# Optimization experiments

Measured on AMD Instinct MI355X. Metric: run time of the kernel, lower is better.

## Reference

```python
import jax, jax.numpy as jnp
import numpy as np

PRE_NMS_THRESH = 0.05
PRE_NMS_TOP_N = 1000
NMS_THRESH = 0.6
FPN_POST_NMS_TOP_N = 100
MIN_SIZE = 0
OFFSET = 10000.0  # per-class coordinate offset for batched per-class NMS
NEG = -1e9


def bilinear_resize(x, out_h, out_w):
    # x: [H, W, C] -> [out_h, out_w, C], matches torch interpolate(align_corners=False)
    H, W, _ = x.shape
    def grid(in_size, out_size):
        scale = in_size / out_size
        src = (jnp.arange(out_size, dtype=jnp.float32) + 0.5) * scale - 0.5
        src = jnp.clip(src, 0.0, in_size - 1.0)
        i0 = jnp.floor(src).astype(jnp.int32)
        i1 = jnp.minimum(i0 + 1, in_size - 1)
        lam = src - i0.astype(jnp.float32)
        return i0, i1, lam
    r0, r1, rl = grid(H, out_h)
    c0, c1, cl = grid(W, out_w)
    x = x[r0] * (1.0 - rl)[:, None, None] + x[r1] * rl[:, None, None]
    x = x[:, c0] * (1.0 - cl)[None, :, None] + x[:, c1] * cl[None, :, None]
    return x


def box_iou_plus1(b):
    area = (b[:, 2] - b[:, 0] + 1.0) * (b[:, 3] - b[:, 1] + 1.0)
    lt = jnp.maximum(b[:, None, :2], b[None, :, :2])
    rb = jnp.minimum(b[:, None, 2:], b[None, :, 2:])
    wh = jnp.clip(rb - lt + 1.0, 0.0)
    inter = wh[..., 0] * wh[..., 1]
    union = area[:, None] + area[None, :] - inter
    return inter / jnp.maximum(union, 1e-6)


def _forward(locations, box_cls, box_regression, centerness, box_mask, h, w):
    N, C, H, W = box_cls.shape
    M2 = box_mask.shape[1]
    Mi = int(np.sqrt(M2))
    HW = H * W
    K = PRE_NMS_TOP_N

    cls = jax.nn.sigmoid(box_cls.transpose(0, 2, 3, 1).reshape(N, HW, C))
    reg = box_regression.transpose(0, 2, 3, 1).reshape(N, HW, 4)
    cent = jax.nn.sigmoid(centerness.reshape(N, HW))
    mask = jax.nn.sigmoid(box_mask.transpose(0, 2, 3, 1))  # [N,H,W,M2]

    cand = cls > PRE_NMS_THRESH               # candidates from raw cls scores
    scr = cls * cent[:, :, None]              # centerness-weighted scores

    def per_image(cand_i, scr_i, reg_i, mask_i):
        # --- threshold + per-image topk (fixed K, padded with NEG) ---
        flat = jnp.where(cand_i, scr_i, NEG).reshape(HW * C)
        vals, idx = jax.lax.top_k(flat, K)
        valid = vals > NEG / 2
        loc_idx = idx // C
        labels = idx % C + 1                  # 1-based class labels
        locs = locations[loc_idx]             # [K,2]
        r = reg_i[loc_idx]                    # [K,4]
        boxes = jnp.stack([locs[:, 0] - r[:, 0], locs[:, 1] - r[:, 1],
                           locs[:, 0] + r[:, 2], locs[:, 1] + r[:, 3]], axis=1)
        scores = jnp.sqrt(jnp.where(valid, vals, 1.0)) * valid

        # --- mask paste: mean of upsampled mask over (buggy) box region ---
        up = bilinear_resize(mask_i, h, w)                      # [h,w,M2]
        integ = jnp.pad(jnp.cumsum(jnp.cumsum(up, 0), 1), ((1, 0), (1, 0), (0, 0)))
        bi = boxes.astype(jnp.int32)          # torch .int() truncation
        x1 = jnp.maximum(bi[:, 0], 0); x2 = jnp.minimum(bi[:, 2], h - 1)
        y1 = jnp.maximum(bi[:, 1], 0); y2 = jnp.minimum(bi[:, 3], w - 1)
        # original skip condition is (x1>=x2 or y1>=x2) -- bug replicated; extra
        # y1<y2 guard avoids NaN mean over empty region
        region_ok = (x1 < x2) & (y1 < x2) & (y1 < y2)
        x1c = jnp.clip(x1, 0, h); x2c = jnp.clip(x2, 0, h)
        y1c = jnp.clip(y1, 0, w); y2c = jnp.clip(y2, 0, w)
        s = integ[x2c, y2c] - integ[x1c, y2c] - integ[x2c, y1c] + integ[x1c, y1c]
        area = jnp.maximum((x2c - x1c) * (y2c - y1c), 1).astype(s.dtype)
        prob = ((s / area[:, None]) * region_ok[:, None]).reshape(K, Mi, Mi)

        # --- clip_to_image (x in [0,w-1], y in [0,h-1]) + remove_small_boxes ---
        bx = jnp.stack([jnp.clip(boxes[:, 0], 0, w - 1), jnp.clip(boxes[:, 1], 0, h - 1),
                        jnp.clip(boxes[:, 2], 0, w - 1), jnp.clip(boxes[:, 3], 0, h - 1)], 1)
        ws_ = bx[:, 2] - bx[:, 0] + 1.0
        hs_ = bx[:, 3] - bx[:, 1] + 1.0
        valid = valid & (ws_ >= MIN_SIZE) & (hs_ >= MIN_SIZE)

        # --- per-class greedy NMS via class-offset trick (fixed shape) ---
        nb = bx + (labels.astype(bx.dtype) * OFFSET)[:, None]
        order = jnp.argsort(-jnp.where(valid, scores, -1.0))
        nb_s, sc_s, v_s = nb[order], scores[order], valid[order]
        iou = box_iou_plus1(nb_s)
        rng = jnp.arange(K)
        def step(keep, i):
            ki = keep[i] & v_s[i]
            keep = keep.at[i].set(ki)
            keep = keep & ~(ki & (iou[i] > NMS_THRESH) & (rng > i))
            return keep, None
        keep, _ = jax.lax.scan(step, jnp.ones(K, bool), jnp.arange(K))
        v_final = keep & v_s

        # --- keep fpn_post_nms_top_n highest-scoring survivors ---
        fvals, fidx = jax.lax.top_k(jnp.where(v_final, sc_s, -1.0), FPN_POST_NMS_TOP_N)
        sel = order[fidx]
        vfin = v_final[fidx]
        return (bx[sel], scores[sel] * vfin, labels[sel], prob[sel] * vfin[:, None, None], vfin)

    return jax.vmap(per_image)(cand, scr, reg, mask)


def setup_inputs() -> dict:
    key = jax.random.key(0)
    ks = jax.random.split(key, 4)
    N, C, H, W, M2 = 2, 80, 32, 40, 196
    stride = 8
    ys, xs = jnp.meshgrid(jnp.arange(H), jnp.arange(W), indexing='ij')
    locations = jnp.stack([xs.reshape(-1), ys.reshape(-1)], 1).astype(jnp.float32) * stride + stride // 2
    box_cls = jax.random.normal(ks[0], (N, C, H, W), jnp.float32) - 2.0
    box_regression = jax.random.uniform(ks[1], (N, 4, H, W), jnp.float32) * 60.0 + 4.0
    centerness = jax.random.normal(ks[2], (N, 1, H, W), jnp.float32)
    box_mask = jax.random.normal(ks[3], (N, M2, H, W), jnp.float32)
    return {"locations": locations, "box_cls": box_cls, "box_regression": box_regression,
            "centerness": centerness, "box_mask": box_mask, "image_h": 256, "image_w": 320}


def reference(locations, box_cls, box_regression, centerness, box_mask, image_h, image_w):
    return _forward(locations, box_cls, box_regression, centerness, box_mask, image_h, image_w)
```

## Files before the change

kernel.cpp:

```cpp
#include <hip/hip_runtime.h>

#define DEVI __device__ __forceinline__

constexpr int N_ = 2, C_ = 80, H_ = 32, W_ = 40, HW_ = H_ * W_, HWC_ = HW_ * C_;
constexpr int KTOP = 1000, M2_ = 196;
constexpr int IMH = 256, IMW = 320;
constexpr int NB = 2048;
constexpr int KB = 16;
constexpr int SLICE = HWC_ / KB;
constexpr int BCAP = 2048;
constexpr int GCAP = 4096;

constexpr int O_SC = 800, O_LB = 1000, O_PB = 1200, O_VF = 40400;

DEVI unsigned long long mapd(double v) {
  unsigned long long u = (unsigned long long)__double_as_longlong(v);
  return (u & 0x8000000000000000ull) ? ~u : (u | 0x8000000000000000ull);
}
DEVI double unmapd(unsigned long long k) {
  unsigned long long u = (k & 0x8000000000000000ull) ? (k ^ 0x8000000000000000ull) : ~k;
  return __longlong_as_double((long long)u);
}
DEVI int i0of(int x, int cap) {
  float src = ((float)x + 0.5f) * 0.125f - 0.5f;
  src = fminf(fmaxf(src, 0.f), (float)cap);
  return (int)floorf(src);
}

__global__ __launch_bounds__(1024) void k_pre(const float* cls, const float* cent, const float* bm,
                                              unsigned* ghist, float* msig, float* wr, float* wc) {
  int b = blockIdx.x, tid = threadIdx.x;
  if (b < N_ * KB) {
    __shared__ unsigned hist[NB];
    __shared__ float ce[HW_];
    int n = b >> 4, sb = b & 15;
    size_t base = (size_t)n * HWC_ + (size_t)sb * SLICE;
    for (int j = tid; j < NB; j += 1024) hist[j] = 0;
    for (int j = tid; j < HW_; j += 1024) ce[j] = 1.f / (1.f + expf(-cent[n * HW_ + j]));
    __syncthreads();
    #pragma unroll
    for (int it = 0; it < 7; ++it) {
      int j = it * 1024 + tid;
      if (j < SLICE) {
        float aa = cls[base + j];
        float s = 1.f / (1.f + expf(-aa));
        if (s > 0.0499999f) {
          unsigned key = __float_as_uint(s * ce[j % HW_]);
          int bin = (int)(key >> 16) - 0x3800;
          bin = bin < 0 ? 0 : (bin > NB - 1 ? NB - 1 : bin);
          atomicAdd(&hist[bin], 1u);
        }
      }
    }
    __syncthreads();
    unsigned* gh = ghist + ((size_t)n * KB + sb) * NB;
    for (int j = tid; j < NB; j += 1024) gh[j] = hist[j];
  } else if (b < N_ * KB + 140) {
    __shared__ float tile[4][32][33];
    int g = tid >> 8, sub = tid & 255;
    int tt = (b - N_ * KB) * 4 + g;
    int n = tt / 280, r = tt % 280, rqt = r / 7, ct = r % 7;
    int tx = sub & 31, ty = sub >> 5;
    int rq0 = rqt * 32, c0 = ct * 32;
    for (int i = 0; i < 4; ++i) {
      int cc = c0 + ty + i * 8, rq = rq0 + tx;
      if (cc < M2_) {
        float v = bm[((size_t)n * M2_ + cc) * HW_ + rq];
        tile[g][ty + i * 8][tx] = 1.f / (1.f + expf(-v));
      }
    }
    __syncthreads();
    for (int i = 0; i < 4; ++i) {
      int rq = rq0 + ty + i * 8, cc = c0 + tx;
      if (cc < M2_) msig[((size_t)n * HW_ + rq) * M2_ + cc] = tile[g][tx][ty + i * 8];
    }
  } else {
    int t = tid;
    if (t < H_) {
      int r = t; float acc = 0.f; wr[0 * H_ + r] = 0.f;
      for (int x = 0; x < IMH; ++x) {
        float src = ((float)x + 0.5f) * ((float)H_ / (float)IMH) - 0.5f;
        src = fminf(fmaxf(src, 0.f), (float)(H_ - 1));
        int i0 = (int)floorf(src); int i1 = min(i0 + 1, H_ - 1);
        float lam = src - (float)i0;
        float w = ((r == i0) ? (1.f - lam) : 0.f) + ((r == i1) ? lam : 0.f);
        acc += w; wr[(x + 1) * H_ + r] = acc;
      }
    } else if (t < H_ + W_) {
      int q = t - H_; float acc = 0.f; wc[0 * W_ + q] = 0.f;
      for (int y = 0; y < IMW; ++y) {
        float src = ((float)y + 0.5f) * ((float)W_ / (float)IMW) - 0.5f;
        src = fminf(fmaxf(src, 0.f), (float)(W_ - 1));
        int i0 = (int)floorf(src); int i1 = min(i0 + 1, W_ - 1);
        float lam = src - (float)i0;
        float w = ((q == i0) ? (1.f - lam) : 0.f) + ((q == i1) ? lam : 0.f);
        acc += w; wc[(y + 1) * W_ + q] = acc;
      }
    }
  }
}

__global__ __launch_bounds__(1024) void k_compact(const unsigned* ghist, const float* cls, const float* cent,
                                                  unsigned long long* bufK, unsigned* bufI, unsigned* cntG) {
  __shared__ unsigned wtot[16], wabove[16], sliceCnt[16], sliceOff[17];
  __shared__ unsigned sD, lcnt;
  __shared__ float ce[HW_];
  int b = blockIdx.x, n = b >> 4, sb = b & 15;
  int tid = threadIdx.x, lane = tid & 63, wid = tid >> 6;
  for (int j = tid; j < HW_; j += 1024) ce[j] = 1.f / (1.f + expf(-cent[n * HW_ + j]));
  const unsigned* gh = ghist + (size_t)n * KB * NB;
  unsigned a = 0, bv = 0;
  #pragma unroll
  for (int q = 0; q < KB; ++q) { a += gh[q * NB + 2 * tid]; bv += gh[q * NB + 2 * tid + 1]; }
  if (tid == 0) { sD = 0; lcnt = 0; }
  unsigned s2 = a + bv, suf = s2;
  for (int off = 1; off < 64; off <<= 1) {
    unsigned v = __shfl_down(suf, off);
    if (lane + off < 64) suf += v;
  }
  if (lane == 0) wtot[wid] = suf;
  __syncthreads();
  if (tid == 0) { unsigned acc = 0; for (int w = 15; w >= 0; --w) { wabove[w] = acc; acc += wtot[w]; } }
  __syncthreads();
  unsigned above = (suf - s2) + wabove[wid];
  if (above < 1000u && above + bv >= 1000u) sD = (unsigned)(2 * tid + 1);
  if (above + bv < 1000u && above + bv + a >= 1000u) sD = (unsigned)(2 * tid);
  __syncthreads();
  unsigned D = sD;
  unsigned Dg = (D > 0) ? D - 1 : 0;
  {
    unsigned acc = 0;
    for (int bin = (int)Dg + lane; bin < NB; bin += 64) acc += gh[wid * NB + bin];
    for (int off = 32; off; off >>= 1) acc += __shfl_down(acc, off);
    if (lane == 0) sliceCnt[wid] = acc;
  }
  __syncthreads();
  if (tid == 0) {
    unsigned acc = 0;
    for (int q = 0; q < KB; ++q) { sliceOff[q] = acc; acc += sliceCnt[q]; }
    sliceOff[KB] = acc;
    if (sb == 0) cntG[n] = acc;
  }
  __syncthreads();
  unsigned myStart = sliceOff[sb];
  size_t gbase = (size_t)n * HWC_ + (size_t)sb * SLICE;
  for (int it = 0; it < 7; ++it) {
    int j = it * 1024 + tid;
    bool win = false; float aa = 0.f;
    if (j < SLICE) {
      aa = cls[gbase + j];
      float s = 1.f / (1.f + expf(-aa));
      if (s > 0.0499999f) {
        unsigned key = __float_as_uint(s * ce[j % HW_]);
        int bin = (int)(key >> 16) - 0x3800;
        bin = bin < 0 ? 0 : (bin > NB - 1 ? NB - 1 : bin);
        win = ((unsigned)bin >= Dg);
      }
    }
    unsigned long long mb = __ballot(win);
    if (mb) {
      int lead = __builtin_ctzll(mb);
      unsigned offw = 0;
      if (lane == lead) offw = atomicAdd(&lcnt, (unsigned)__popcll(mb));
      offw = (unsigned)__shfl((int)offw, lead);
      if (win) {
        unsigned pos = myStart + offw + (unsigned)__popcll(mb & ((1ull << lane) - 1ull));
        if (pos < (unsigned)GCAP) {
          int hw = j % HW_, c = sb * 5 + j / HW_;
          double ss = 1.0 / (1.0 + exp(-(double)aa));
          double ced = 1.0 / (1.0 + exp(-(double)cent[n * HW_ + hw]));
          double v = (ss > 0.05) ? ss * ced : -1e9;
          bufK[(size_t)n * GCAP + pos] = mapd(v);
          bufI[(size_t)n * GCAP + pos] = (unsigned)(hw * C_ + c);
        }
      }
    }
  }
}

struct RankSh {
  unsigned long long K[BCAP];
  unsigned I[BCAP];
  unsigned short eb[BCAP];
  unsigned short ord[BCAP];
  unsigned bh[NB], bs[NB], cur[NB];
  unsigned long long Ks[1024];
  unsigned Is[1024];
  unsigned wtot[16], wabove[16];
};

__global__ __launch_bounds__(1024) void k_rankdec(const unsigned long long* bufK, const unsigned* bufI,
                                                  const unsigned* cntG, const float* loc, const float* breg,
                                                  double* bxd, double* scd, int* lab, int* vld, int* rg,
                                                  unsigned* keepg) {
  __shared__ RankSh sh;
  int n = blockIdx.x, tid = threadIdx.x, lane = tid & 63, wid = tid >> 6;
  keepg[n * 1024 + tid] = 0;
  int G = (int)cntG[n]; if (G > BCAP) G = BCAP;
  for (int j = tid; j < NB; j += 1024) sh.bh[j] = 0;
  for (int p = tid; p < G; p += 1024) {
    sh.K[p] = bufK[(size_t)n * GCAP + p];
    sh.I[p] = bufI[(size_t)n * GCAP + p];
  }
  __syncthreads();
  for (int p = tid; p < G; p += 1024) {
    double v = unmapd(sh.K[p]);
    int bb = 0;
    if (v > 0.0) {
      unsigned kb = __float_as_uint((float)v);
      bb = (int)(kb >> 16) - 0x3800;
      bb = bb < 0 ? 0 : (bb > NB - 1 ? NB - 1 : bb);
    }
    sh.eb[p] = (unsigned short)bb;
    atomicAdd(&sh.bh[bb], 1u);
  }
  __syncthreads();
  {
    unsigned a2 = sh.bh[2 * tid], b2 = sh.bh[2 * tid + 1];
    unsigned s3 = a2 + b2, suf2 = s3;
    for (int off = 1; off < 64; off <<= 1) {
      unsigned v = __shfl_down(suf2, off);
      if (lane + off < 64) suf2 += v;
    }
    if (lane == 0) sh.wtot[wid] = suf2;
    __syncthreads();
    if (tid == 0) { unsigned acc = 0; for (int w = 15; w >= 0; --w) { sh.wabove[w] = acc; acc += sh.wtot[w]; } }
    __syncthreads();
    unsigned above2 = (suf2 - s3) + sh.wabove[wid];
    sh.bs[2 * tid + 1] = above2;  sh.cur[2 * tid + 1] = above2;
    sh.bs[2 * tid] = above2 + b2; sh.cur[2 * tid] = above2 + b2;
  }
  __syncthreads();
  for (int p = tid; p < G; p += 1024) {
    unsigned p2 = atomicAdd(&sh.cur[sh.eb[p]], 1u);
    sh.ord[p2] = (unsigned short)p;
  }
  __syncthreads();
  for (int p = tid; p < G; p += 1024) {
    int bb = sh.eb[p];
    unsigned lo = sh.bs[bb], len = sh.bh[bb];
    unsigned long long k1 = sh.K[p]; unsigned i1 = sh.I[p];
    unsigned r = lo;
    for (unsigned q = lo; q < lo + len; ++q) {
      int j = sh.ord[q];
      unsigned long long kj = sh.K[j]; unsigned ij = sh.I[j];
      if ((kj > k1) || (kj == k1 && ij < i1)) ++r;
    }
    if (r < 1024u) { sh.Ks[r] = k1; sh.Is[r] = i1; }
  }
  for (int j = G + tid; j < 1024; j += 1024) { sh.Ks[j] = 0ull; sh.Is[j] = 0xFFFFFFFFu; }
  __syncthreads();
  if (tid < KTOP) {
    unsigned long long key = sh.Ks[tid];
    unsigned idx = sh.Is[tid];
    double v = unmapd(key);
    int valid = (v > -5e8) && (idx < (unsigned)HWC_);
    if (idx >= (unsigned)HWC_) idx = 0;
    int hw = (int)(idx / C_), c = (int)(idx % C_);
    double lx = (double)loc[hw * 2 + 0], ly = (double)loc[hw * 2 + 1];
    const float* rg4 = breg + (size_t)n * 4 * HW_;
    double r0 = (double)rg4[0 * HW_ + hw], r1 = (double)rg4[1 * HW_ + hw];
    double r2 = (double)rg4[2 * HW_ + hw], r3 = (double)rg4[3 * HW_ + hw];
    double b0 = lx - r0, b1 = ly - r1, b2 = lx + r2, b3 = ly + r3;
    double sc = valid ? sqrt(v) : 0.0;
    int bi0 = (int)b0, bi1 = (int)b1, bi2 = (int)b2, bi3 = (int)b3;
    int x1 = max(bi0, 0), x2 = min(bi2, IMH - 1), y1 = max(bi1, 0), y2 = min(bi3, IMW - 1);
    int rok = (x1 < x2) && (y1 < x2) && (y1 < y2);
    int x1c = min(max(x1, 0), IMH), x2c = min(max(x2, 0), IMH);
    int y1c = min(max(y1, 0), IMW), y2c = min(max(y2, 0), IMW);
    int area = max((x2c - x1c) * (y2c - y1c), 1);
    double c0 = fmin(fmax(b0, 0.0), (double)(IMW - 1));
    double c1 = fmin(fmax(b1, 0.0), (double)(IMH - 1));
    double c2 = fmin(fmax(b2, 0.0), (double)(IMW - 1));
    double c3 = fmin(fmax(b3, 0.0), (double)(IMH - 1));
    size_t base = (size_t)n * 1024 + tid;
    bxd[base * 4 + 0] = c0; bxd[base * 4 + 1] = c1; bxd[base * 4 + 2] = c2; bxd[base * 4 + 3] = c3;
    scd[base] = sc; lab[base] = c + 1; vld[base] = valid;
    int* r8 = rg + base * 8;
    r8[0] = x1c; r8[1] = x2c; r8[2] = y1c; r8[3] = y2c; r8[4] = area; r8[5] = rok;
  }
}

__global__ void k_nms(const double* bxd, const int* lab, const int* vld, unsigned* keepg) {
  int cls = blockIdx.x + 1, n = blockIdx.y, tid = threadIdx.x;
  __shared__ int mk[KTOP];
  __shared__ double mb0[KTOP], mb1[KTOP], mb2[KTOP], mb3[KTOP], ma[KTOP];
  __shared__ unsigned char kept[KTOP];
  int m = 0;
  for (int base = 0; base < KTOP; base += 64) {
    int t = base + tid;
    bool pred = (t < KTOP) && (lab[n * 1024 + t] == cls) && (vld[n * 1024 + t] != 0);
    unsigned long long bb = __ballot(pred);
    if (pred) {
      int pos = m + (int)__popcll(bb & ((1ull << tid) - 1ull));
      mk[pos] = t;
      const double* p = bxd + ((size_t)n * 1024 + t) * 4;
      double b0 = p[0], b1 = p[1], b2 = p[2], b3 = p[3];
      mb0[pos] = b0; mb1[pos] = b1; mb2[pos] = b2; mb3[pos] = b3;
      ma[pos] = (b2 - b0 + 1.0) * (b3 - b1 + 1.0);
      kept[pos] = 1;
    }
    m += (int)__popcll(bb);
  }
  __syncthreads();
  for (int i = 0; i < m; ++i) {
    if (kept[i]) {
      double x1 = mb0[i], y1 = mb1[i], x2 = mb2[i], y2 = mb3[i], ai = ma[i];
      for (int j = i + 1 + tid; j < m; j += 64) {
        double ltx = fmax(x1, mb0[j]), lty = fmax(y1, mb1[j]);
        double rbx = fmin(x2, mb2[j]), rby = fmin(y2, mb3[j]);
        double iw = fmax(rbx - ltx + 1.0, 0.0), ih = fmax(rby - lty + 1.0, 0.0);
        double inter = iw * ih;
        double uni = ai + ma[j] - inter;
        if (inter / fmax(uni, 1e-6) > 0.6) kept[j] = 0;
      }
    }
    __syncthreads();
  }
  for (int i = tid; i < m; i += 64) keepg[n * 1024 + mk[i]] = (unsigned)kept[i];
}

__global__ __launch_bounds__(256) void k_finish(const unsigned* keepg, const double* bxd,
                                                const double* scd, const int* lab, const int* rg,
                                                const float* msig, const float* wr, const float* wc,
                                                float* out) {
  int t = blockIdx.x, n = blockIdx.y, tid = threadIdx.x, lane = tid & 63, wid = tid >> 6;
  __shared__ int lsel[100], lvf[100];
  __shared__ unsigned woff[4]; __shared__ unsigned sS;
  __shared__ float A[H_], B[W_];

  int i0 = tid * 4;
  unsigned ff[4]; int lc = 0;
  for (int j = 0; j < 4; ++j) {
    int i = i0 + j;
    ff[j] = (i < KTOP) ? keepg[n * 1024 + i] : 0u;
    lc += (int)ff[j];
  }
  unsigned pre = (unsigned)lc;
  for (int off = 1; off < 64; off <<= 1) {
    unsigned v = __shfl_up(pre, off);
    if (lane >= off) pre += v;
  }
  if (lane == 63) woff[wid] = pre;
  __syncthreads();
  if (tid == 0) { unsigned acc = 0; for (int w = 0; w < 4; ++w) { unsigned tmp = woff[w]; woff[w] = acc; acc += tmp; } sS = acc; }
  __syncthreads();
  int kpre = (int)(woff[wid] + pre - (unsigned)lc);
  int S = (int)sS;
  for (int j = 0; j < 4; ++j) {
    int i = i0 + j;
    if (i < KTOP) {
      if (ff[j]) { if (kpre < 100) { lsel[kpre] = i; lvf[kpre] = 1; } kpre++; }
      else { int slot = S + (i - kpre); if (slot < 100) { lsel[slot] = i; lvf[slot] = 0; } }
    }
  }
  __syncthreads();

  int k = lsel[t], vf = lvf[t];
  if (tid == 0) {
    const double* bb = bxd + ((size_t)n * 1024 + k) * 4;
    out[(n * 100 + t) * 4 + 0] = (float)bb[0];
    out[(n * 100 + t) * 4 + 1] = (float)bb[1];
    out[(n * 100 + t) * 4 + 2] = (float)bb[2];
    out[(n * 100 + t) * 4 + 3] = (float)bb[3];
    out[O_SC + n * 100 + t] = vf ? (float)scd[n * 1024 + k] : 0.f;
    out[O_LB + n * 100 + t] = (float)lab[n * 1024 + k];
    out[O_VF + n * 100 + t] = (float)vf;
  }
  const int* r8 = rg + ((size_t)n * 1024 + k) * 8;
  int x1c = r8[0], x2c = r8[1], y1c = r8[2], y2c = r8[3], area = r8[4], rok = r8[5];
  if (tid < H_) A[tid] = wr[x2c * H_ + tid] - wr[x1c * H_ + tid];
  else if (tid < H_ + W_) { int q = tid - H_; B[q] = wc[y2c * W_ + q] - wc[y1c * W_ + q]; }
  __syncthreads();
  if (tid < M2_) {
    float acc = 0.f;
    if (rok && vf) {
      int rlo = i0of(x1c, H_ - 1);
      int rhi = min(i0of(x2c - 1, H_ - 1) + 1, H_ - 1);
      int qlo = i0of(y1c, W_ - 1);
      int qhi = min(i0of(y2c - 1, W_ - 1) + 1, W_ - 1);
      for (int r = rlo; r <= rhi; ++r) {
        float ar = A[r];
        const float* mrow = msig + ((size_t)((n * H_ + r) * W_ + qlo)) * M2_ + tid;
        float rs = 0.f;
        #pragma unroll 4
        for (int q = qlo; q <= qhi; ++q) { rs += B[q] * mrow[0]; mrow += M2_; }
        acc += ar * rs;
      }
      acc /= (float)area;
    }
    out[O_PB + (size_t)(n * 100 + t) * M2_ + tid] = acc;
  }
}

extern "C" void kernel_launch(void* const* d_in, const int* in_sizes, int n_in,
                              void* d_out, int out_size, void* d_ws, size_t ws_size,
                              hipStream_t stream) {
  (void)in_sizes; (void)n_in; (void)out_size; (void)ws_size;
  const float* locations = (const float*)d_in[0];
  const float* box_cls   = (const float*)d_in[1];
  const float* box_reg   = (const float*)d_in[2];
  const float* cent      = (const float*)d_in[3];
  const float* box_mask  = (const float*)d_in[4];
  float* out = (float*)d_out;

  char* ws = (char*)d_ws;
  size_t off = 0;
  auto alloc = [&](size_t bytes) -> void* {
    void* p = ws + off;
    off = (off + bytes + 255) & ~(size_t)255;
    return p;
  };
  unsigned* ghist          = (unsigned*)alloc((size_t)N_ * KB * NB * 4);
  unsigned long long* bufK = (unsigned long long*)alloc((size_t)N_ * GCAP * 8);
  unsigned* bufI           = (unsigned*)alloc((size_t)N_ * GCAP * 4);
  unsigned* cntG           = (unsigned*)alloc(16 * 4);
  double* bxd              = (double*)alloc((size_t)N_ * 1024 * 4 * 8);
  double* scd              = (double*)alloc((size_t)N_ * 1024 * 8);
  int* lab                 = (int*)alloc((size_t)N_ * 1024 * 4);
  int* vld                 = (int*)alloc((size_t)N_ * 1024 * 4);
  int* rg                  = (int*)alloc((size_t)N_ * 1024 * 8 * 4);
  unsigned* keepg          = (unsigned*)alloc((size_t)N_ * 1024 * 4);
  float* msig              = (float*)alloc((size_t)N_ * HW_ * M2_ * 4);
  float* wr                = (float*)alloc((size_t)(IMH + 1) * H_ * 4);
  float* wc                = (float*)alloc((size_t)(IMW + 1) * W_ * 4);

  k_pre<<<N_ * KB + 140 + 1, 1024, 0, stream>>>(box_cls, cent, box_mask, ghist, msig, wr, wc);
  k_compact<<<N_ * KB, 1024, 0, stream>>>(ghist, box_cls, cent, bufK, bufI, cntG);
  k_rankdec<<<N_, 1024, 0, stream>>>(bufK, bufI, cntG, locations, box_reg,
                                     bxd, scd, lab, vld, rg, keepg);
  k_nms<<<dim3(C_, N_), 64, 0, stream>>>(bxd, lab, vld, keepg);
  k_finish<<<dim3(100, N_), 256, 0, stream>>>(keepg, bxd, scd, lab, rg, msig, wr, wc, out);
}
```

Baseline: 91.70 us.

## Merge five kernels into two using inter-block flag barriers

Fuses histogram, compaction and rank/decode into one kernel whose blocks synchronize through global spin-wait flags instead of kernel boundaries. NMS and the finishing mask-pooling stage are merged into a second kernel, also using flags. This removes three kernel launches and their gaps. The cost is spin-waiting that depends on all cooperating blocks being co-resident, plus flag reset bookkeeping that could deadlock or race if residency or ordering assumptions fail.

```diff
diff --git a/kernel.cpp b/kernel.cpp
--- a/kernel.cpp
+++ b/kernel.cpp
@@ -10,6 +10,7 @@
 constexpr int SLICE = HWC_ / KB;
 constexpr int BCAP = 2048;
 constexpr int GCAP = 4096;
+constexpr unsigned MAGIC = 0x5EEDFACEu;
 
 constexpr int O_SC = 800, O_LB = 1000, O_PB = 1200, O_VF = 40400;
 
@@ -27,36 +28,229 @@
   return (int)floorf(src);
 }
 
-__global__ __launch_bounds__(1024) void k_pre(const float* cls, const float* cent, const float* bm,
-                                              unsigned* ghist, float* msig, float* wr, float* wc) {
-  int b = blockIdx.x, tid = threadIdx.x;
+DEVI unsigned aload(unsigned* p) { return atomicAdd(p, 0u); }
+
+struct SliceSh {
+  unsigned hist[NB];
+  float ce[HW_];
+  unsigned wtot[16], wabove[16], sliceCnt[16], sliceOff[17];
+  unsigned sD, lcnt;
+};
+struct RankSh {
+  unsigned long long K[BCAP];
+  unsigned I[BCAP];
+  unsigned short eb[BCAP];
+  unsigned short ord[BCAP];
+  unsigned bh[NB], bs[NB], cur[NB];
+  unsigned long long Ks[1024];
+  unsigned Is[1024];
+  unsigned wtot[16], wabove[16];
+};
+struct MaskSh { float tile[4][32][33]; };
+union ShA { SliceSh s; RankSh r; MaskSh m; };
+
+__global__ __launch_bounds__(1024) void k_a(const float* cls, const float* cent, const float* bm,
+                                            const float* loc, const float* breg,
+                                            unsigned* ghist, unsigned long long* bufK, unsigned* bufI,
+                                            double* bxd, double* scd, int* lab, int* vld, int* rg,
+                                            unsigned* keepg, float* msig, float* wr, float* wc,
+                                            unsigned* flags) {
+  __shared__ ShA sh;
+  int b = blockIdx.x, tid = threadIdx.x, lane = tid & 63, wid = tid >> 6;
+
   if (b < N_ * KB) {
-    __shared__ unsigned hist[NB];
-    __shared__ float ce[HW_];
     int n = b >> 4, sb = b & 15;
-    size_t base = (size_t)n * HWC_ + (size_t)sb * SLICE;
-    for (int j = tid; j < NB; j += 1024) hist[j] = 0;
-    for (int j = tid; j < HW_; j += 1024) ce[j] = 1.f / (1.f + expf(-cent[n * HW_ + j]));
+    size_t gbase = (size_t)n * HWC_ + (size_t)sb * SLICE;
+    for (int j = tid; j < NB; j += 1024) sh.s.hist[j] = 0;
+    for (int j = tid; j < HW_; j += 1024) sh.s.ce[j] = 1.f / (1.f + expf(-cent[n * HW_ + j]));
     __syncthreads();
     #pragma unroll
     for (int it = 0; it < 7; ++it) {
       int j = it * 1024 + tid;
       if (j < SLICE) {
-        float aa = cls[base + j];
+        float aa = cls[gbase + j];
         float s = 1.f / (1.f + expf(-aa));
         if (s > 0.0499999f) {
-          unsigned key = __float_as_uint(s * ce[j % HW_]);
+          unsigned key = __float_as_uint(s * sh.s.ce[j % HW_]);
           int bin = (int)(key >> 16) - 0x3800;
           bin = bin < 0 ? 0 : (bin > NB - 1 ? NB - 1 : bin);
-          atomicAdd(&hist[bin], 1u);
+          atomicAdd(&sh.s.hist[bin], 1u);
         }
       }
     }
     __syncthreads();
     unsigned* gh = ghist + ((size_t)n * KB + sb) * NB;
-    for (int j = tid; j < NB; j += 1024) gh[j] = hist[j];
+    for (int j = tid; j < NB; j += 1024) gh[j] = sh.s.hist[j];
+    __threadfence();
+    if (tid == 0) atomicExch(&flags[n * 16 + sb], MAGIC);
+    if (tid == 0) { for (int q = 0; q < 16; ++q) while (aload(&flags[n * 16 + q]) != MAGIC) {} }
+    __syncthreads();
+    __threadfence();
+    {
+      const unsigned* ghn = ghist + (size_t)n * KB * NB;
+      unsigned a = 0, bv = 0;
+      #pragma unroll
+      for (int q = 0; q < KB; ++q) { a += ghn[q * NB + 2 * tid]; bv += ghn[q * NB + 2 * tid + 1]; }
+      if (tid == 0) { sh.s.sD = 0; sh.s.lcnt = 0; }
+      unsigned s2 = a + bv, suf = s2;
+      for (int off = 1; off < 64; off <<= 1) {
+        unsigned v = __shfl_down(suf, off);
+        if (lane + off < 64) suf += v;
+      }
+      if (lane == 0) sh.s.wtot[wid] = suf;
+      __syncthreads();
+      if (tid == 0) { unsigned acc = 0; for (int w = 15; w >= 0; --w) { sh.s.wabove[w] = acc; acc += sh.s.wtot[w]; } }
+      __syncthreads();
+      unsigned above = (suf - s2) + sh.s.wabove[wid];
+      if (above < 1000u && above + bv >= 1000u) sh.s.sD = (unsigned)(2 * tid + 1);
+      if (above + bv < 1000u && above + bv + a >= 1000u) sh.s.sD = (unsigned)(2 * tid);
+      __syncthreads();
+      unsigned D = sh.s.sD;
+      unsigned Dg = (D > 0) ? D - 1 : 0;
+      {
+        unsigned acc = 0;
+        for (int bin = (int)Dg + lane; bin < NB; bin += 64) acc += ghn[wid * NB + bin];
+        for (int off = 32; off; off >>= 1) acc += __shfl_down(acc, off);
+        if (lane == 0) sh.s.sliceCnt[wid] = acc;
+      }
+      __syncthreads();
+      if (tid == 0) {
+        unsigned acc = 0;
+        for (int q = 0; q < KB; ++q) { sh.s.sliceOff[q] = acc; acc += sh.s.sliceCnt[q]; }
+        sh.s.sliceOff[KB] = acc;
+      }
+      __syncthreads();
+      unsigned myStart = sh.s.sliceOff[sb];
+      for (int it = 0; it < 7; ++it) {
+        int j = it * 1024 + tid;
+        bool win = false; float aa = 0.f;
+        if (j < SLICE) {
+          aa = cls[gbase + j];
+          float s = 1.f / (1.f + expf(-aa));
+          if (s > 0.0499999f) {
+            unsigned key = __float_as_uint(s * sh.s.ce[j % HW_]);
+            int bin = (int)(key >> 16) - 0x3800;
+            bin = bin < 0 ? 0 : (bin > NB - 1 ? NB - 1 : bin);
+            win = ((unsigned)bin >= Dg);
+          }
+        }
+        unsigned long long mb = __ballot(win);
+        if (mb) {
+          int lead = __builtin_ctzll(mb);
+          unsigned offw = 0;
+          if (lane == lead) offw = atomicAdd(&sh.s.lcnt, (unsigned)__popcll(mb));
+          offw = (unsigned)__shfl((int)offw, lead);
+          if (win) {
+            unsigned pos = myStart + offw + (unsigned)__popcll(mb & ((1ull << lane) - 1ull));
+            if (pos < (unsigned)GCAP) {
+              int hw = j % HW_, c = sb * 5 + j / HW_;
+              double ss = 1.0 / (1.0 + exp(-(double)aa));
+              double ced = 1.0 / (1.0 + exp(-(double)cent[n * HW_ + hw]));
+              double v = (ss > 0.05) ? ss * ced : -1e9;
+              bufK[(size_t)n * GCAP + pos] = mapd(v);
+              bufI[(size_t)n * GCAP + pos] = (unsigned)(hw * C_ + c);
+            }
+          }
+        }
+      }
+    }
+    int G = (int)sh.s.sliceOff[KB];
+    __threadfence();
+    if (tid == 0) atomicExch(&flags[32 + n * 16 + sb], MAGIC);
+    if (sb != 0) return;
+    if (tid == 0) { for (int q = 0; q < 16; ++q) while (aload(&flags[32 + n * 16 + q]) != MAGIC) {} }
+    __syncthreads();
+    __threadfence();
+    if (G > BCAP) G = BCAP;
+    for (int j = tid; j < NB; j += 1024) sh.r.bh[j] = 0;
+    for (int p = tid; p < G; p += 1024) {
+      sh.r.K[p] = bufK[(size_t)n * GCAP + p];
+      sh.r.I[p] = bufI[(size_t)n * GCAP + p];
+    }
+    __syncthreads();
+    for (int p = tid; p < G; p += 1024) {
+      double v = unmapd(sh.r.K[p]);
+      int bb = 0;
+      if (v > 0.0) {
+        unsigned kb = __float_as_uint((float)v);
+        bb = (int)(kb >> 16) - 0x3800;
+        bb = bb < 0 ? 0 : (bb > NB - 1 ? NB - 1 : bb);
+      }
+      sh.r.eb[p] = (unsigned short)bb;
+      atomicAdd(&sh.r.bh[bb], 1u);
+    }
+    __syncthreads();
+    {
+      unsigned a2 = sh.r.bh[2 * tid], b2 = sh.r.bh[2 * tid + 1];
+      unsigned s3 = a2 + b2, suf2 = s3;
+      for (int off = 1; off < 64; off <<= 1) {
+        unsigned v = __shfl_down(suf2, off);
+        if (lane + off < 64) suf2 += v;
+      }
+      if (lane == 0) sh.r.wtot[wid] = suf2;
+      __syncthreads();
+      if (tid == 0) { unsigned acc = 0; for (int w = 15; w >= 0; --w) { sh.r.wabove[w] = acc; acc += sh.r.wtot[w]; } }
+      __syncthreads();
+      unsigned above2 = (suf2 - s3) + sh.r.wabove[wid];
+      sh.r.bs[2 * tid + 1] = above2;  sh.r.cur[2 * tid + 1] = above2;
+      sh.r.bs[2 * tid] = above2 + b2; sh.r.cur[2 * tid] = above2 + b2;
+    }
+    __syncthreads();
+    for (int p = tid; p < G; p += 1024) {
+      unsigned p2 = atomicAdd(&sh.r.cur[sh.r.eb[p]], 1u);
+      sh.r.ord[p2] = (unsigned short)p;
+    }
+    __syncthreads();
+    for (int p = tid; p < G; p += 1024) {
+      int bb = sh.r.eb[p];
+      unsigned lo = sh.r.bs[bb], len = sh.r.bh[bb];
+      unsigned long long k1 = sh.r.K[p]; unsigned i1 = sh.r.I[p];
+      unsigned r = lo;
+      for (unsigned q = lo; q < lo + len; ++q) {
+        int j = sh.r.ord[q];
+        unsigned long long kj = sh.r.K[j]; unsigned ij = sh.r.I[j];
+        if ((kj > k1) || (kj == k1 && ij < i1)) ++r;
+      }
+      if (r < 1024u) { sh.r.Ks[r] = k1; sh.r.Is[r] = i1; }
+    }
+    for (int j = G + tid; j < 1024; j += 1024) { sh.r.Ks[j] = 0ull; sh.r.Is[j] = 0xFFFFFFFFu; }
+    __syncthreads();
+    if (tid < KTOP) {
+      unsigned long long key = sh.r.Ks[tid];
+      unsigned idx = sh.r.Is[tid];
+      double v = unmapd(key);
+      int valid = (v > -5e8) && (idx < (unsigned)HWC_);
+      if (idx >= (unsigned)HWC_) idx = 0;
+      int hw = (int)(idx / C_), c = (int)(idx % C_);
+      double lx = (double)loc[hw * 2 + 0], ly = (double)loc[hw * 2 + 1];
+      const float* rg4 = breg + (size_t)n * 4 * HW_;
+      double r0 = (double)rg4[0 * HW_ + hw], r1 = (double)rg4[1 * HW_ + hw];
+      double r2 = (double)rg4[2 * HW_ + hw], r3 = (double)rg4[3 * HW_ + hw];
+      double b0 = lx - r0, b1 = ly - r1, b2 = lx + r2, b3 = ly + r3;
+      double sc = valid ? sqrt(v) : 0.0;
+      int bi0 = (int)b0, bi1 = (int)b1, bi2 = (int)b2, bi3 = (int)b3;
+      int x1 = max(bi0, 0), x2 = min(bi2, IMH - 1), y1 = max(bi1, 0), y2 = min(bi3, IMW - 1);
+      int rok = (x1 < x2) && (y1 < x2) && (y1 < y2);
+      int x1c = min(max(x1, 0), IMH), x2c = min(max(x2, 0), IMH);
+      int y1c = min(max(y1, 0), IMW), y2c = min(max(y2, 0), IMW);
+      int area = max((x2c - x1c) * (y2c - y1c), 1);
+      double c0 = fmin(fmax(b0, 0.0), (double)(IMW - 1));
+      double c1 = fmin(fmax(b1, 0.0), (double)(IMH - 1));
+      double c2 = fmin(fmax(b2, 0.0), (double)(IMW - 1));
+      double c3 = fmin(fmax(b3, 0.0), (double)(IMH - 1));
+      size_t base = (size_t)n * 1024 + tid;
+      bxd[base * 4 + 0] = c0; bxd[base * 4 + 1] = c1; bxd[base * 4 + 2] = c2; bxd[base * 4 + 3] = c3;
+      scd[base] = sc; lab[base] = c + 1; vld[base] = valid;
+      int* r8 = rg + base * 8;
+      r8[0] = x1c; r8[1] = x2c; r8[2] = y1c; r8[3] = y2c; r8[4] = area; r8[5] = rok;
+    }
+    for (int j = tid; j < 1024; j += 1024) keepg[n * 1024 + j] = 0;
+    __syncthreads();
+    if (tid == 0) {
+      flags[64 + n] = 0;
+      for (int q = 0; q < 16; ++q) { flags[n * 16 + q] = 0; flags[32 + n * 16 + q] = 0; }
+    }
   } else if (b < N_ * KB + 140) {
-    __shared__ float tile[4][32][33];
     int g = tid >> 8, sub = tid & 255;
     int tt = (b - N_ * KB) * 4 + g;
     int n = tt / 280, r = tt % 280, rqt = r / 7, ct = r % 7;
@@ -66,13 +260,13 @@
       int cc = c0 + ty + i * 8, rq = rq0 + tx;
       if (cc < M2_) {
         float v = bm[((size_t)n * M2_ + cc) * HW_ + rq];
-        tile[g][ty + i * 8][tx] = 1.f / (1.f + expf(-v));
+        sh.m.tile[g][ty + i * 8][tx] = 1.f / (1.f + expf(-v));
       }
     }
     __syncthreads();
     for (int i = 0; i < 4; ++i) {
       int rq = rq0 + ty + i * 8, cc = c0 + tx;
-      if (cc < M2_) msig[((size_t)n * HW_ + rq) * M2_ + cc] = tile[g][tx][ty + i * 8];
+      if (cc < M2_) msig[((size_t)n * HW_ + rq) * M2_ + cc] = sh.m.tile[g][tx][ty + i * 8];
     }
   } else {
     int t = tid;
@@ -100,296 +294,144 @@
   }
 }
 
-__global__ __launch_bounds__(1024) void k_compact(const unsigned* ghist, const float* cls, const float* cent,
-                                                  unsigned long long* bufK, unsigned* bufI, unsigned* cntG) {
-  __shared__ unsigned wtot[16], wabove[16], sliceCnt[16], sliceOff[17];
-  __shared__ unsigned sD, lcnt;
-  __shared__ float ce[HW_];
-  int b = blockIdx.x, n = b >> 4, sb = b & 15;
-  int tid = threadIdx.x, lane = tid & 63, wid = tid >> 6;
-  for (int j = tid; j < HW_; j += 1024) ce[j] = 1.f / (1.f + expf(-cent[n * HW_ + j]));
-  const unsigned* gh = ghist + (size_t)n * KB * NB;
-  unsigned a = 0, bv = 0;
-  #pragma unroll
-  for (int q = 0; q < KB; ++q) { a += gh[q * NB + 2 * tid]; bv += gh[q * NB + 2 * tid + 1]; }
-  if (tid == 0) { sD = 0; lcnt = 0; }
-  unsigned s2 = a + bv, suf = s2;
-  for (int off = 1; off < 64; off <<= 1) {
-    unsigned v = __shfl_down(suf, off);
-    if (lane + off < 64) suf += v;
-  }
-  if (lane == 0) wtot[wid] = suf;
-  __syncthreads();
-  if (tid == 0) { unsigned acc = 0; for (int w = 15; w >= 0; --w) { wabove[w] = acc; acc += wtot[w]; } }
-  __syncthreads();
-  unsigned above = (suf - s2) + wabove[wid];
-  if (above < 1000u && above + bv >= 1000u) sD = (unsigned)(2 * tid + 1);
-  if (above + bv < 1000u && above + bv + a >= 1000u) sD = (unsigned)(2 * tid);
-  __syncthreads();
-  unsigned D = sD;
-  unsigned Dg = (D > 0) ? D - 1 : 0;
-  {
-    unsigned acc = 0;
-    for (int bin = (int)Dg + lane; bin < NB; bin += 64) acc += gh[wid * NB + bin];
-    for (int off = 32; off; off >>= 1) acc += __shfl_down(acc, off);
-    if (lane == 0) sliceCnt[wid] = acc;
-  }
-  __syncthreads();
-  if (tid == 0) {
-    unsigned acc = 0;
-    for (int q = 0; q < KB; ++q) { sliceOff[q] = acc; acc += sliceCnt[q]; }
-    sliceOff[KB] = acc;
-    if (sb == 0) cntG[n] = acc;
-  }
-  __syncthreads();
-  unsigned myStart = sliceOff[sb];
-  size_t gbase = (size_t)n * HWC_ + (size_t)sb * SLICE;
-  for (int it = 0; it < 7; ++it) {
-    int j = it * 1024 + tid;
-    bool win = false; float aa = 0.f;
-    if (j < SLICE) {
-      aa = cls[gbase + j];
-      float s = 1.f / (1.f + expf(-aa));
-      if (s > 0.0499999f) {
-        unsigned key = __float_as_uint(s * ce[j % HW_]);
-        int bin = (int)(key >> 16) - 0x3800;
-        bin = bin < 0 ? 0 : (bin > NB - 1 ? NB - 1 : bin);
-        win = ((unsigned)bin >= Dg);
-      }
-    }
-    unsigned long long mb = __ballot(win);
-    if (mb) {
-      int lead = __builtin_ctzll(mb);
-      unsigned offw = 0;
-      if (lane == lead) offw = atomicAdd(&lcnt, (unsigned)__popcll(mb));
-      offw = (unsigned)__shfl((int)offw, lead);
-      if (win) {
-        unsigned pos = myStart + offw + (unsigned)__popcll(mb & ((1ull << lane) - 1ull));
-        if (pos < (unsigned)GCAP) {
-          int hw = j % HW_, c = sb * 5 + j / HW_;
-          double ss = 1.0 / (1.0 + exp(-(double)aa));
-          double ced = 1.0 / (1.0 + exp(-(double)cent[n * HW_ + hw]));
-          double v = (ss > 0.05) ? ss * ced : -1e9;
-          bufK[(size_t)n * GCAP + pos] = mapd(v);
-          bufI[(size_t)n * GCAP + pos] = (unsigned)(hw * C_ + c);
-        }
-      }
-    }
-  }
-}
-
-struct RankSh {
-  unsigned long long K[BCAP];
-  unsigned I[BCAP];
-  unsigned short eb[BCAP];
-  unsigned short ord[BCAP];
-  unsigned bh[NB], bs[NB], cur[NB];
-  unsigned long long Ks[1024];
-  unsigned Is[1024];
-  unsigned wtot[16], wabove[16];
-};
-
-__global__ __launch_bounds__(1024) void k_rankdec(const unsigned long long* bufK, const unsigned* bufI,
-                                                  const unsigned* cntG, const float* loc, const float* breg,
-                                                  double* bxd, double* scd, int* lab, int* vld, int* rg,
-                                                  unsigned* keepg) {
-  __shared__ RankSh sh;
-  int n = blockIdx.x, tid = threadIdx.x, lane = tid & 63, wid = tid >> 6;
-  keepg[n * 1024 + tid] = 0;
-  int G = (int)cntG[n]; if (G > BCAP) G = BCAP;
-  for (int j = tid; j < NB; j += 1024) sh.bh[j] = 0;
-  for (int p = tid; p < G; p += 1024) {
-    sh.K[p] = bufK[(size_t)n * GCAP + p];
-    sh.I[p] = bufI[(size_t)n * GCAP + p];
-  }
-  __syncthreads();
-  for (int p = tid; p < G; p += 1024) {
-    double v = unmapd(sh.K[p]);
-    int bb = 0;
-    if (v > 0.0) {
-      unsigned kb = __float_as_uint((float)v);
-      bb = (int)(kb >> 16) - 0x3800;
-      bb = bb < 0 ? 0 : (bb > NB - 1 ? NB - 1 : bb);
-    }
-    sh.eb[p] = (unsigned short)bb;
-    atomicAdd(&sh.bh[bb], 1u);
-  }
-  __syncthreads();
-  {
-    unsigned a2 = sh.bh[2 * tid], b2 = sh.bh[2 * tid + 1];
-    unsigned s3 = a2 + b2, suf2 = s3;
+struct NmsSh { double bx[128][5]; unsigned short ml[128]; };
+struct FinSh { int lsel[100], lvf[100]; unsigned woff[4]; unsigned sS; float A[H_], Bw[W_]; };
+union ShB { NmsSh nm; FinSh fn; };
+
+__global__ __launch_bounds__(256) void k_b(const double* bxd, const double* scd, const int* lab,
+                                           const int* vld, const int* rg, unsigned* keepg,
+                                           const float* msig, const float* wr, const float* wc,
+                                           unsigned* flags, float* out) {
+  __shared__ ShB sh;
+  int b = blockIdx.x, tid = threadIdx.x, lane = tid & 63, wid = tid >> 6;
+
+  if (b < N_ * C_) {
+    int n = b / C_, cls_ = b % C_ + 1;
+    if (tid < 64) {
+      int m = 0;
+      for (int ch = 0; ch < 16; ++ch) {
+        int e = ch * 64 + lane;
+        bool pred = (e < KTOP) && vld[n * 1024 + e] && (lab[n * 1024 + e] == cls_);
+        unsigned long long bb = __ballot(pred);
+        if (pred) {
+          int pos = m + (int)__popcll(bb & ((1ull << lane) - 1ull));
+          if (pos < 128) {
+            const double* p = bxd + ((size_t)n * 1024 + e) * 4;
+            double b0 = p[0], b1 = p[1], b2 = p[2], b3 = p[3];
+            sh.nm.bx[pos][0] = b0; sh.nm.bx[pos][1] = b1; sh.nm.bx[pos][2] = b2; sh.nm.bx[pos][3] = b3;
+            sh.nm.bx[pos][4] = (b2 - b0 + 1.0) * (b3 - b1 + 1.0);
+            sh.nm.ml[pos] = (unsigned short)e;
+          }
+        }
+        m += (int)__popcll(bb);
+      }
+      if (m > 128) m = 128;
+      __builtin_amdgcn_wave_barrier();
+      unsigned long long k0 = (m >= 64) ? ~0ull : ((1ull << m) - 1ull);
+      unsigned long long k1m = (m > 64) ? ((m >= 128) ? ~0ull : ((1ull << (m - 64)) - 1ull)) : 0ull;
+      for (int i = 0; i < m; ++i) {
+        bool alive = (i < 64) ? ((k0 >> i) & 1ull) : ((k1m >> (i - 64)) & 1ull);
+        if (!alive) continue;
+        double x1 = sh.nm.bx[i][0], y1 = sh.nm.bx[i][1], x2 = sh.nm.bx[i][2], y2 = sh.nm.bx[i][3], ai = sh.nm.bx[i][4];
+        {
+          int j = lane;
+          bool ok = (j < m) && (j > i);
+          int jj = ok ? j : 0;
+          double u1 = sh.nm.bx[jj][0], v1 = sh.nm.bx[jj][1], u2 = sh.nm.bx[jj][2], v2 = sh.nm.bx[jj][3], aj = sh.nm.bx[jj][4];
+          double ltx = fmax(x1, u1), lty = fmax(y1, v1), rbx = fmin(x2, u2), rby = fmin(y2, v2);
+          double iw = fmax(rbx - ltx + 1.0, 0.0), ih = fmax(rby - lty + 1.0, 0.0);
+          double inter = iw * ih, uni = ai + aj - inter;
+          bool sup = ok && (inter / fmax(uni, 1e-6) > 0.6);
+          k0 &= ~__ballot(sup);
+        }
+        if (m > 64) {
+          int j = 64 + lane;
+          bool ok = (j < m) && (j > i);
+          int jj = ok ? j : 0;
+          double u1 = sh.nm.bx[jj][0], v1 = sh.nm.bx[jj][1], u2 = sh.nm.bx[jj][2], v2 = sh.nm.bx[jj][3], aj = sh.nm.bx[jj][4];
+          double ltx = fmax(x1, u1), lty = fmax(y1, v1), rbx = fmin(x2, u2), rby = fmin(y2, v2);
+          double iw = fmax(rbx - ltx + 1.0, 0.0), ih = fmax(rby - lty + 1.0, 0.0);
+          double inter = iw * ih, uni = ai + aj - inter;
+          bool sup = ok && (inter / fmax(uni, 1e-6) > 0.6);
+          k1m &= ~__ballot(sup);
+        }
+      }
+      for (int j = lane; j < m; j += 64) {
+        bool kb2 = (j < 64) ? ((k0 >> j) & 1ull) : ((k1m >> (j - 64)) & 1ull);
+        keepg[n * 1024 + sh.nm.ml[j]] = kb2 ? 1u : 0u;
+      }
+    }
+    __threadfence();
+    if (tid == 0) atomicAdd(&flags[64 + n], 1u);
+  } else {
+    int idx = b - N_ * C_;
+    int n = idx / 100, t = idx % 100;
+    if (tid == 0) { while (aload(&flags[64 + n]) < (unsigned)C_) {} }
+    __syncthreads();
+    __threadfence();
+
+    int i0 = tid * 4;
+    unsigned ff[4]; int lc = 0;
+    for (int j = 0; j < 4; ++j) {
+      int i = i0 + j;
+      ff[j] = (i < KTOP) ? keepg[n * 1024 + i] : 0u;
+      lc += (int)ff[j];
+    }
+    unsigned pre = (unsigned)lc;
     for (int off = 1; off < 64; off <<= 1) {
-      unsigned v = __shfl_down(suf2, off);
-      if (lane + off < 64) suf2 += v;
-    }
-    if (lane == 0) sh.wtot[wid] = suf2;
-    __syncthreads();
-    if (tid == 0) { unsigned acc = 0; for (int w = 15; w >= 0; --w) { sh.wabove[w] = acc; acc += sh.wtot[w]; } }
-    __syncthreads();
-    unsigned above2 = (suf2 - s3) + sh.wabove[wid];
-    sh.bs[2 * tid + 1] = above2;  sh.cur[2 * tid + 1] = above2;
-    sh.bs[2 * tid] = above2 + b2; sh.cur[2 * tid] = above2 + b2;
-  }
-  __syncthreads();
-  for (int p = tid; p < G; p += 1024) {
-    unsigned p2 = atomicAdd(&sh.cur[sh.eb[p]], 1u);
-    sh.ord[p2] = (unsigned short)p;
-  }
-  __syncthreads();
-  for (int p = tid; p < G; p += 1024) {
-    int bb = sh.eb[p];
-    unsigned lo = sh.bs[bb], len = sh.bh[bb];
-    unsigned long long k1 = sh.K[p]; unsigned i1 = sh.I[p];
-    unsigned r = lo;
-    for (unsigned q = lo; q < lo + len; ++q) {
-      int j = sh.ord[q];
-      unsigned long long kj = sh.K[j]; unsigned ij = sh.I[j];
-      if ((kj > k1) || (kj == k1 && ij < i1)) ++r;
-    }
-    if (r < 1024u) { sh.Ks[r] = k1; sh.Is[r] = i1; }
-  }
-  for (int j = G + tid; j < 1024; j += 1024) { sh.Ks[j] = 0ull; sh.Is[j] = 0xFFFFFFFFu; }
-  __syncthreads();
-  if (tid < KTOP) {
-    unsigned long long key = sh.Ks[tid];
-    unsigned idx = sh.Is[tid];
-    double v = unmapd(key);
-    int valid = (v > -5e8) && (idx < (unsigned)HWC_);
-    if (idx >= (unsigned)HWC_) idx = 0;
-    int hw = (int)(idx / C_), c = (int)(idx % C_);
-    double lx = (double)loc[hw * 2 + 0], ly = (double)loc[hw * 2 + 1];
-    const float* rg4 = breg + (size_t)n * 4 * HW_;
-    double r0 = (double)rg4[0 * HW_ + hw], r1 = (double)rg4[1 * HW_ + hw];
-    double r2 = (double)rg4[2 * HW_ + hw], r3 = (double)rg4[3 * HW_ + hw];
-    double b0 = lx - r0, b1 = ly - r1, b2 = lx + r2, b3 = ly + r3;
-    double sc = valid ? sqrt(v) : 0.0;
-    int bi0 = (int)b0, bi1 = (int)b1, bi2 = (int)b2, bi3 = (int)b3;
-    int x1 = max(bi0, 0), x2 = min(bi2, IMH - 1), y1 = max(bi1, 0), y2 = min(bi3, IMW - 1);
-    int rok = (x1 < x2) && (y1 < x2) && (y1 < y2);
-    int x1c = min(max(x1, 0), IMH), x2c = min(max(x2, 0), IMH);
-    int y1c = min(max(y1, 0), IMW), y2c = min(max(y2, 0), IMW);
-    int area = max((x2c - x1c) * (y2c - y1c), 1);
-    double c0 = fmin(fmax(b0, 0.0), (double)(IMW - 1));
-    double c1 = fmin(fmax(b1, 0.0), (double)(IMH - 1));
-    double c2 = fmin(fmax(b2, 0.0), (double)(IMW - 1));
-    double c3 = fmin(fmax(b3, 0.0), (double)(IMH - 1));
-    size_t base = (size_t)n * 1024 + tid;
-    bxd[base * 4 + 0] = c0; bxd[base * 4 + 1] = c1; bxd[base * 4 + 2] = c2; bxd[base * 4 + 3] = c3;
-    scd[base] = sc; lab[base] = c + 1; vld[base] = valid;
-    int* r8 = rg + base * 8;
-    r8[0] = x1c; r8[1] = x2c; r8[2] = y1c; r8[3] = y2c; r8[4] = area; r8[5] = rok;
-  }
-}
-
-__global__ void k_nms(const double* bxd, const int* lab, const int* vld, unsigned* keepg) {
-  int cls = blockIdx.x + 1, n = blockIdx.y, tid = threadIdx.x;
-  __shared__ int mk[KTOP];
-  __shared__ double mb0[KTOP], mb1[KTOP], mb2[KTOP], mb3[KTOP], ma[KTOP];
-  __shared__ unsigned char kept[KTOP];
-  int m = 0;
-  for (int base = 0; base < KTOP; base += 64) {
-    int t = base + tid;
-    bool pred = (t < KTOP) && (lab[n * 1024 + t] == cls) && (vld[n * 1024 + t] != 0);
-    unsigned long long bb = __ballot(pred);
-    if (pred) {
-      int pos = m + (int)__popcll(bb & ((1ull << tid) - 1ull));
-      mk[pos] = t;
-      const double* p = bxd + ((size_t)n * 1024 + t) * 4;
-      double b0 = p[0], b1 = p[1], b2 = p[2], b3 = p[3];
-      mb0[pos] = b0; mb1[pos] = b1; mb2[pos] = b2; mb3[pos] = b3;
-      ma[pos] = (b2 - b0 + 1.0) * (b3 - b1 + 1.0);
-      kept[pos] = 1;
-    }
-    m += (int)__popcll(bb);
-  }
-  __syncthreads();
-  for (int i = 0; i < m; ++i) {
-    if (kept[i]) {
-      double x1 = mb0[i], y1 = mb1[i], x2 = mb2[i], y2 = mb3[i], ai = ma[i];
-      for (int j = i + 1 + tid; j < m; j += 64) {
-        double ltx = fmax(x1, mb0[j]), lty = fmax(y1, mb1[j]);
-        double rbx = fmin(x2, mb2[j]), rby = fmin(y2, mb3[j]);
-        double iw = fmax(rbx - ltx + 1.0, 0.0), ih = fmax(rby - lty + 1.0, 0.0);
-        double inter = iw * ih;
-        double uni = ai + ma[j] - inter;
-        if (inter / fmax(uni, 1e-6) > 0.6) kept[j] = 0;
-      }
-    }
-    __syncthreads();
-  }
-  for (int i = tid; i < m; i += 64) keepg[n * 1024 + mk[i]] = (unsigned)kept[i];
-}
-
-__global__ __launch_bounds__(256) void k_finish(const unsigned* keepg, const double* bxd,
-                                                const double* scd, const int* lab, const int* rg,
-                                                const float* msig, const float* wr, const float* wc,
-                                                float* out) {
-  int t = blockIdx.x, n = blockIdx.y, tid = threadIdx.x, lane = tid & 63, wid = tid >> 6;
-  __shared__ int lsel[100], lvf[100];
-  __shared__ unsigned woff[4]; __shared__ unsigned sS;
-  __shared__ float A[H_], B[W_];
-
-  int i0 = tid * 4;
-  unsigned ff[4]; int lc = 0;
-  for (int j = 0; j < 4; ++j) {
-    int i = i0 + j;
-    ff[j] = (i < KTOP) ? keepg[n * 1024 + i] : 0u;
-    lc += (int)ff[j];
-  }
-  unsigned pre = (unsigned)lc;
-  for (int off = 1; off < 64; off <<= 1) {
-    unsigned v = __shfl_up(pre, off);
-    if (lane >= off) pre += v;
-  }
-  if (lane == 63) woff[wid] = pre;
-  __syncthreads();
-  if (tid == 0) { unsigned acc = 0; for (int w = 0; w < 4; ++w) { unsigned tmp = woff[w]; woff[w] = acc; acc += tmp; } sS = acc; }
-  __syncthreads();
-  int kpre = (int)(woff[wid] + pre - (unsigned)lc);
-  int S = (int)sS;
-  for (int j = 0; j < 4; ++j) {
-    int i = i0 + j;
-    if (i < KTOP) {
-      if (ff[j]) { if (kpre < 100) { lsel[kpre] = i; lvf[kpre] = 1; } kpre++; }
-      else { int slot = S + (i - kpre); if (slot < 100) { lsel[slot] = i; lvf[slot] = 0; } }
-    }
-  }
-  __syncthreads();
-
-  int k = lsel[t], vf = lvf[t];
-  if (tid == 0) {
-    const double* bb = bxd + ((size_t)n * 1024 + k) * 4;
-    out[(n * 100 + t) * 4 + 0] = (float)bb[0];
-    out[(n * 100 + t) * 4 + 1] = (float)bb[1];
-    out[(n * 100 + t) * 4 + 2] = (float)bb[2];
-    out[(n * 100 + t) * 4 + 3] = (float)bb[3];
-    out[O_SC + n * 100 + t] = vf ? (float)scd[n * 1024 + k] : 0.f;
-    out[O_LB + n * 100 + t] = (float)lab[n * 1024 + k];
-    out[O_VF + n * 100 + t] = (float)vf;
-  }
-  const int* r8 = rg + ((size_t)n * 1024 + k) * 8;
-  int x1c = r8[0], x2c = r8[1], y1c = r8[2], y2c = r8[3], area = r8[4], rok = r8[5];
-  if (tid < H_) A[tid] = wr[x2c * H_ + tid] - wr[x1c * H_ + tid];
-  else if (tid < H_ + W_) { int q = tid - H_; B[q] = wc[y2c * W_ + q] - wc[y1c * W_ + q]; }
-  __syncthreads();
-  if (tid < M2_) {
-    float acc = 0.f;
-    if (rok && vf) {
-      int rlo = i0of(x1c, H_ - 1);
-      int rhi = min(i0of(x2c - 1, H_ - 1) + 1, H_ - 1);
-      int qlo = i0of(y1c, W_ - 1);
-      int qhi = min(i0of(y2c - 1, W_ - 1) + 1, W_ - 1);
-      for (int r = rlo; r <= rhi; ++r) {
-        float ar = A[r];
-        const float* mrow = msig + ((size_t)((n * H_ + r) * W_ + qlo)) * M2_ + tid;
-        float rs = 0.f;
-        #pragma unroll 4
-        for (int q = qlo; q <= qhi; ++q) { rs += B[q] * mrow[0]; mrow += M2_; }
-        acc += ar * rs;
-      }
-      acc /= (float)area;
-    }
-    out[O_PB + (size_t)(n * 100 + t) * M2_ + tid] = acc;
+      unsigned v = __shfl_up(pre, off);
+      if (lane >= off) pre += v;
+    }
+    if (lane == 63) sh.fn.woff[wid] = pre;
+    __syncthreads();
+    if (tid == 0) { unsigned acc = 0; for (int w = 0; w < 4; ++w) { unsigned tmp = sh.fn.woff[w]; sh.fn.woff[w] = acc; acc += tmp; } sh.fn.sS = acc; }
+    __syncthreads();
+    int kpre = (int)(sh.fn.woff[wid] + pre - (unsigned)lc);
+    int S = (int)sh.fn.sS;
+    for (int j = 0; j < 4; ++j) {
+      int i = i0 + j;
+      if (i < KTOP) {
+        if (ff[j]) { if (kpre < 100) { sh.fn.lsel[kpre] = i; sh.fn.lvf[kpre] = 1; } kpre++; }
+        else { int slot = S + (i - kpre); if (slot < 100) { sh.fn.lsel[slot] = i; sh.fn.lvf[slot] = 0; } }
+      }
+    }
+    __syncthreads();
+
+    int k = sh.fn.lsel[t], vf = sh.fn.lvf[t];
+    if (tid == 0) {
+      const double* bb = bxd + ((size_t)n * 1024 + k) * 4;
+      out[(n * 100 + t) * 4 + 0] = (float)bb[0];
+      out[(n * 100 + t) * 4 + 1] = (float)bb[1];
+      out[(n * 100 + t) * 4 + 2] = (float)bb[2];
+      out[(n * 100 + t) * 4 + 3] = (float)bb[3];
+      out[O_SC + n * 100 + t] = vf ? (float)scd[n * 1024 + k] : 0.f;
+      out[O_LB + n * 100 + t] = (float)lab[n * 1024 + k];
+      out[O_VF + n * 100 + t] = (float)vf;
+    }
+    const int* r8 = rg + ((size_t)n * 1024 + k) * 8;
+    int x1c = r8[0], x2c = r8[1], y1c = r8[2], y2c = r8[3], area = r8[4], rok = r8[5];
+    if (tid < H_) sh.fn.A[tid] = wr[x2c * H_ + tid] - wr[x1c * H_ + tid];
+    else if (tid < H_ + W_) { int q = tid - H_; sh.fn.Bw[q] = wc[y2c * W_ + q] - wc[y1c * W_ + q]; }
+    __syncthreads();
+    if (tid < M2_) {
+      float acc = 0.f;
+      if (rok && vf) {
+        int rlo = i0of(x1c, H_ - 1);
+        int rhi = min(i0of(x2c - 1, H_ - 1) + 1, H_ - 1);
+        int qlo = i0of(y1c, W_ - 1);
+        int qhi = min(i0of(y2c - 1, W_ - 1) + 1, W_ - 1);
+        for (int r = rlo; r <= rhi; ++r) {
+          float ar = sh.fn.A[r];
+          const float* mrow = msig + ((size_t)((n * H_ + r) * W_ + qlo)) * M2_ + tid;
+          float rs = 0.f;
+          #pragma unroll 4
+          for (int q = qlo; q <= qhi; ++q) { rs += sh.fn.Bw[q] * mrow[0]; mrow += M2_; }
+          acc += ar * rs;
+        }
+        acc /= (float)area;
+      }
+      out[O_PB + (size_t)(n * 100 + t) * M2_ + tid] = acc;
+    }
   }
 }
 
@@ -414,7 +456,6 @@
   unsigned* ghist          = (unsigned*)alloc((size_t)N_ * KB * NB * 4);
   unsigned long long* bufK = (unsigned long long*)alloc((size_t)N_ * GCAP * 8);
   unsigned* bufI           = (unsigned*)alloc((size_t)N_ * GCAP * 4);
-  unsigned* cntG           = (unsigned*)alloc(16 * 4);
   double* bxd              = (double*)alloc((size_t)N_ * 1024 * 4 * 8);
   double* scd              = (double*)alloc((size_t)N_ * 1024 * 8);
   int* lab                 = (int*)alloc((size_t)N_ * 1024 * 4);
@@ -424,11 +465,11 @@
   float* msig              = (float*)alloc((size_t)N_ * HW_ * M2_ * 4);
   float* wr                = (float*)alloc((size_t)(IMH + 1) * H_ * 4);
   float* wc                = (float*)alloc((size_t)(IMW + 1) * W_ * 4);
-
-  k_pre<<<N_ * KB + 140 + 1, 1024, 0, stream>>>(box_cls, cent, box_mask, ghist, msig, wr, wc);
-  k_compact<<<N_ * KB, 1024, 0, stream>>>(ghist, box_cls, cent, bufK, bufI, cntG);
-  k_rankdec<<<N_, 1024, 0, stream>>>(bufK, bufI, cntG, locations, box_reg,
-                                     bxd, scd, lab, vld, rg, keepg);
-  k_nms<<<dim3(C_, N_), 64, 0, stream>>>(bxd, lab, vld, keepg);
-  k_finish<<<dim3(100, N_), 256, 0, stream>>>(keepg, bxd, scd, lab, rg, msig, wr, wc, out);
-}
+  unsigned* flags          = (unsigned*)alloc(128 * 4);
+
+  k_a<<<N_ * KB + 140 + 1, 1024, 0, stream>>>(box_cls, cent, box_mask, locations, box_reg,
+                                              ghist, bufK, bufI, bxd, scd, lab, vld, rg,
+                                              keepg, msig, wr, wc, flags);
+  k_b<<<N_ * C_ + N_ * 100, 256, 0, stream>>>(bxd, scd, lab, vld, rg, keepg,
+                                              msig, wr, wc, flags, out);
+}
```

New measurement: 127.8 us. 1.39x slower.
